# Performance work log

Hardware: AMD Instinct MI355X
Metric: run time of the kernel (lower is better)

## Reference

```python
import jax, jax.numpy as jnp
import numpy as np

B, DIN, DH, DOUT = 256, 784, 512, 10


def _softplus(x):
    # matches torch.log(1.0 + torch.exp(x)) exactly
    return jnp.log(1.0 + jnp.exp(x))


def _kl(w_mu, w_sigma_sp, size_in):
    # compute_kl_loss(w_mu, diag_embed(softplus(w_sigma))) without materializing diag
    # w_mu: (in, out), w_sigma_sp: (out, in)
    trace = jnp.sum(w_sigma_sp, axis=1)            # (out,)
    mu_sq = jnp.sum(w_mu * w_mu, axis=0)           # (out,)
    logdet = jnp.sum(jnp.log(w_sigma_sp), axis=1)  # slogdet of diag = sum log diag
    return 0.5 * jnp.sum(trace + mu_sq - size_in - logdet)


def setup_inputs() -> dict:
    key = jax.random.key(0)
    ks = jax.random.split(key, 9)
    inp = {
        "x": jax.random.normal(ks[0], (B, DIN, 1), dtype=jnp.float32),
        "w_mu1": 5e-5 * jax.random.normal(ks[1], (DIN, DH), dtype=jnp.float32),
        "w_sigma1": jax.random.uniform(ks[2], (DH, DIN), minval=-12.0, maxval=-2.0, dtype=jnp.float32),
        "b_mu1": 5e-5 * jax.random.normal(ks[3], (DH, 1), dtype=jnp.float32),
        "b_sigma1": jax.random.uniform(ks[4], (DH,), minval=-12.0, maxval=-2.0, dtype=jnp.float32),
        "w_mu2": 5e-5 * jax.random.normal(ks[5], (DH, DOUT), dtype=jnp.float32),
        "w_sigma2": jax.random.uniform(ks[6], (DOUT, DH), minval=-12.0, maxval=-2.0, dtype=jnp.float32),
        "b_mu2": 5e-5 * jax.random.normal(ks[7], (DOUT, 1), dtype=jnp.float32),
        "b_sigma2": jax.random.uniform(ks[8], (DOUT,), minval=-12.0, maxval=-2.0, dtype=jnp.float32),
    }
    return inp


def reference(x, w_mu1, w_sigma1, b_mu1, b_sigma1, w_mu2, w_sigma2, b_mu2, b_sigma2):
    batch = x.shape[0]
    eye_h = jnp.eye(DH, dtype=x.dtype)
    eye_o = jnp.eye(DOUT, dtype=x.dtype)

    # ---- RVLinearlayer 1 (sigma_in = None) ----
    xv = x[..., 0]                                   # (B, DIN)
    mu1 = jnp.einsum('io,bi->bo', w_mu1, xv)[:, :, None] + b_mu1   # (B, DH, 1)
    Ws1 = _softplus(w_sigma1)                        # (DH, DIN)
    quad1 = jnp.einsum('hi,bi->bh', Ws1, xv * xv)    # mu_in^T diag(Ws) mu_in per unit
    sigma1 = quad1[:, :, None] * eye_h + jnp.diag(_softplus(b_sigma1))  # (B, DH, DH)
    kl1 = _kl(w_mu1, Ws1, DIN)

    # ---- RVNonLinearFunc (ReLU) ----
    mu2 = jax.nn.relu(mu1)                           # (B, DH, 1)
    g = (mu1[..., 0] > 0).astype(x.dtype)            # Heaviside grad of relu
    sigma2 = sigma1 * (g[:, :, None] * g[:, None, :])

    # ---- RVLinearlayer 2 (with sigma_in) ----
    m2v = mu2[..., 0]                                # (B, DH)
    mu3 = jnp.einsum('ho,bh->bo', w_mu2, m2v)[:, :, None] + b_mu2   # (B, DOUT, 1)
    Ws2 = _softplus(w_sigma2)                        # (DOUT, DH)
    quad2 = jnp.einsum('oh,bh->bo', Ws2, m2v * m2v)  # (B, DOUT)
    # faithful replication of W_Sigma.view(out,-1) @ sigma_in.view(-1,B) then .view(B,out)
    Sflat = sigma2.reshape(DH * DH, batch)           # same row-major view as torch
    diag_rows = Sflat[jnp.arange(DH) * (DH + 1)]     # rows of the diag positions, (DH, B)
    tr = (Ws2 @ diag_rows).reshape(batch, DOUT)      # (out,B) -> row-major (B,out)
    mid = jnp.einsum('ho,bhk,kp->bop', w_mu2, sigma2, w_mu2)  # w_mu2^T Sigma w_mu2
    sigma3 = (tr[:, :, None] * eye_o + mid + quad2[:, :, None] * eye_o
              + jnp.diag(_softplus(b_sigma2)))       # (B, DOUT, DOUT)
    kl2 = _kl(w_mu2, Ws2, DH)

    # ---- RVSoftmax ----
    p = jax.nn.softmax(mu3[..., 0], axis=1)          # (B, DOUT)
    jac = p[:, :, None] * eye_o - p[:, :, None] * p[:, None, :]  # diag(p) - p p^T
    Sigma_out = jnp.einsum('bij,bjk,blk->bil', jac, sigma3, jac)

    return p, Sigma_out, kl1 + kl2
```

## Files before the change

kernel.cpp:

```cpp
#include <hip/hip_runtime.h>
#include <math.h>

#define BATCH 256
#define DIN 784
#define DH 512
#define DOUT 10
#define SPLITS 28
#define KSPL 28

__device__ __forceinline__ float softplus(float x) {
  return __logf(1.0f + __expf(x));
}

__global__ __launch_bounds__(256) void gemm1_kernel(
    const float* __restrict__ x, const float* __restrict__ w_mu1,
    const float* __restrict__ w_sigma1, const float* __restrict__ w_mu2,
    const float* __restrict__ w_sigma2, float* __restrict__ mu_part,
    float* __restrict__ q_part, float* __restrict__ kl_part) {
  __shared__ float xs[64][KSPL];
  __shared__ float wmt[KSPL][68];
  __shared__ float wst[KSPL][68];
  __shared__ float rlds[4];
  const int t = threadIdx.x;
  const int h0 = blockIdx.x * 64;
  const int b0 = blockIdx.y * 64;
  const int s = blockIdx.z;
  const int i0 = s * KSPL;
  const int hl = (t & 15) * 4;
  const int bg = (t >> 4) * 4;

  for (int f = t; f < 64 * KSPL; f += 256) {
    const int bb = f / KSPL, kk = f - bb * KSPL;
    xs[bb][kk] = x[(b0 + bb) * DIN + i0 + kk];
  }
  for (int f = t; f < KSPL * 64; f += 256) {
    const int kk = f >> 6, hh = f & 63;
    wmt[kk][hh] = w_mu1[(i0 + kk) * DH + h0 + hh];
  }
  for (int f = t; f < 64 * KSPL; f += 256) {
    const int hh = f / KSPL, kk = f - hh * KSPL;
    wst[kk][hh] = softplus(w_sigma1[(h0 + hh) * DIN + i0 + kk]);
  }
  __syncthreads();

  float mu[4][4], qq[4][4];
#pragma unroll
  for (int j = 0; j < 4; j++)
#pragma unroll
    for (int i = 0; i < 4; i++) {
      mu[j][i] = 0.f;
      qq[j][i] = 0.f;
    }

#pragma unroll 7
  for (int kk = 0; kk < KSPL; kk += 2) {
    const float4 wm0 = *(const float4*)&wmt[kk][hl];
    const float4 wm1 = *(const float4*)&wmt[kk + 1][hl];
    const float4 ws0 = *(const float4*)&wst[kk][hl];
    const float4 ws1 = *(const float4*)&wst[kk + 1][hl];
    const float* wm0a = (const float*)&wm0;
    const float* wm1a = (const float*)&wm1;
    const float* ws0a = (const float*)&ws0;
    const float* ws1a = (const float*)&ws1;
#pragma unroll
    for (int j = 0; j < 4; j++) {
      const float2 xv = *(const float2*)&xs[bg + j][kk];
      const float xx = xv.x, xy = xv.y;
      const float x2 = xx * xx, y2 = xy * xy;
#pragma unroll
      for (int i = 0; i < 4; i++) {
        mu[j][i] = fmaf(wm0a[i], xx, mu[j][i]);
        mu[j][i] = fmaf(wm1a[i], xy, mu[j][i]);
        qq[j][i] = fmaf(ws0a[i], x2, qq[j][i]);
        qq[j][i] = fmaf(ws1a[i], y2, qq[j][i]);
      }
    }
  }

  const int h = h0 + hl;
  const size_t base = (size_t)s * (BATCH * DH);
#pragma unroll
  for (int j = 0; j < 4; j++) {
    const size_t row = base + (size_t)(b0 + bg + j) * DH + h;
    *(float4*)&mu_part[row] =
        make_float4(mu[j][0], mu[j][1], mu[j][2], mu[j][3]);
    *(float4*)&q_part[row] =
        make_float4(qq[j][0], qq[j][1], qq[j][2], qq[j][3]);
  }

  float kl = 0.f;
  int slot = -1;
  if (blockIdx.y == 0) {
    for (int f = t; f < KSPL * 64; f += 256) {
      const int kk = f >> 6, hh = f & 63;
      const float sv = wst[kk][hh];
      kl += sv - __logf(sv);
    }
    slot = blockIdx.x * 28 + s;
  } else if (blockIdx.y == 1) {
    for (int f = t; f < KSPL * 64; f += 256) {
      const int kk = f >> 6, hh = f & 63;
      const float wv = wmt[kk][hh];
      kl = fmaf(wv, wv, kl);
    }
    slot = 224 + blockIdx.x * 28 + s;
  } else if (blockIdx.y == 2 && blockIdx.x == 0 && s < 16) {
    for (int idx = s * 320 + t; idx < s * 320 + 320; idx += 256) {
      const float sv = softplus(w_sigma2[idx]);
      const float wv = w_mu2[idx];
      kl += sv - __logf(sv);
      kl = fmaf(wv, wv, kl);
    }
    slot = 448 + s;
  }

  for (int off = 32; off > 0; off >>= 1) kl += __shfl_down(kl, off);
  const int lane = t & 63, wv = t >> 6;
  if (lane == 0) rlds[wv] = kl;
  __syncthreads();
  if (t == 0 && slot >= 0)
    kl_part[slot] = rlds[0] + rlds[1] + rlds[2] + rlds[3];
}

__global__ __launch_bounds__(512) void layer2_kernel(
    const float* __restrict__ mu_part, const float* __restrict__ q_part,
    const float* __restrict__ b_mu1, const float* __restrict__ b_sigma1,
    const float* __restrict__ w_mu2, const float* __restrict__ w_sigma2,
    const float* __restrict__ b_mu2, const float* __restrict__ b_sigma2,
    const float* __restrict__ kl_part, float* __restrict__ out_p,
    float* __restrict__ out_sigma, float* __restrict__ out_kl) {
  const int b = blockIdx.x, t = threadIdx.x;
  __shared__ float smuA[DH], sqA[DH], smuB[DH], sqB[DH];
  __shared__ float4 trp[10][7];
  __shared__ float red[8][75];
  __shared__ float fin[75];
  __shared__ float mu3[10], pvec[10], trv[10], spb2[10];
  __shared__ float sig[10][10], Tm[10][10], cs[10], rs[10];
  __shared__ float klred[8];

  {
    const int half = t >> 8;
    const int arr = (t >> 7) & 1;
    const int h4 = (t & 127) * 4;
    const float* srcbase = (arr == 0 ? mu_part : q_part);
    const float4* src = (const float4*)(srcbase + (size_t)b * DH + h4);
    float4 a = make_float4(0.f, 0.f, 0.f, 0.f);
#pragma unroll
    for (int s2 = half * 14; s2 < half * 14 + 14; s2++) {
      const float4 v = src[(size_t)s2 * (BATCH * DH / 4)];
      a.x += v.x;
      a.y += v.y;
      a.z += v.z;
      a.w += v.w;
    }
    float* dst = (half == 0 ? (arr == 0 ? smuA : sqA)
                            : (arr == 0 ? smuB : sqB));
    *(float4*)&dst[h4] = a;
  }

  if (t < 70) {
    const int o = t / 7, g = t % 7;
    const int cc = (b * 10 + o) & 255;
    float mua = 0.f, qa = 0.f, mub = 0.f, qb = 0.f;
#pragma unroll
    for (int s2 = 4 * g; s2 < 4 * g + 4; s2++) {
      const size_t base = (size_t)s2 * (BATCH * DH) + (size_t)cc * DH;
      mua += mu_part[base + cc];
      qa += q_part[base + cc];
      mub += mu_part[base + 256 + cc];
      qb += q_part[base + 256 + cc];
    }
    trp[o][g] = make_float4(mua, qa, mub, qb);
  }
  __syncthreads();

  const int h = t;
  float m2h, d2h;
  {
    const float ma = smuA[h] + smuB[h] + b_mu1[h];
    m2h = ma > 0.f ? ma : 0.f;
    d2h = ma > 0.f ? (sqA[h] + sqB[h] + softplus(b_sigma1[h])) : 0.f;
  }

  float acc[75];
#pragma unroll
  for (int i = 0; i < 75; i++) acc[i] = 0.f;
  {
    const float msq = m2h * m2h;
    float wrow[10];
#pragma unroll
    for (int o = 0; o < 10; o++) wrow[o] = w_mu2[h * 10 + o];
#pragma unroll
    for (int o = 0; o < 10; o++) {
      acc[o] = fmaf(wrow[o], m2h, acc[o]);
      acc[10 + o] = fmaf(softplus(w_sigma2[o * DH + h]), msq, acc[10 + o]);
    }
    int idx = 20;
#pragma unroll
    for (int o = 0; o < 10; o++) {
      const float wd = wrow[o] * d2h;
#pragma unroll
      for (int p = o; p < 10; p++) {
        acc[idx] = fmaf(wd, wrow[p], acc[idx]);
        idx++;
      }
    }
  }

  const int lane = t & 63, wv = t >> 6;
#pragma unroll
  for (int j = 0; j < 75; j++) {
    float v = acc[j];
    for (int off = 32; off > 0; off >>= 1) v += __shfl_down(v, off);
    if (lane == 0) red[wv][j] = v;
  }
  __syncthreads();
  if (t < 75) {
    float v = 0.f;
#pragma unroll
    for (int w = 0; w < 8; w++) v += red[w][t];
    fin[t] = v;
  }
  __syncthreads();

  if (t < 10) {
    mu3[t] = fin[t] + b_mu2[t];
    spb2[t] = softplus(b_sigma2[t]);
    const int c0 = b * 10 + t;
    const int o2 = c0 >> 8, cc = c0 & 255;
    float mua = b_mu1[cc], qa = 0.f;
    float mub = b_mu1[256 + cc], qb = 0.f;
#pragma unroll
    for (int g = 0; g < 7; g++) {
      const float4 v = trp[t][g];
      mua += v.x;
      qa += v.y;
      mub += v.z;
      qb += v.w;
    }
    const float d2aa = mua > 0.f ? (qa + softplus(b_sigma1[cc])) : 0.f;
    const float d2bb = mub > 0.f ? (qb + softplus(b_sigma1[256 + cc])) : 0.f;
    trv[t] = softplus(w_sigma2[o2 * DH + 2 * cc]) * d2aa +
             softplus(w_sigma2[o2 * DH + 2 * cc + 1]) * d2bb;
  }
  __syncthreads();

  if (t == 0) {
    float mx = mu3[0];
#pragma unroll
    for (int o = 1; o < 10; o++) mx = fmaxf(mx, mu3[o]);
    float e[10], se = 0.f;
#pragma unroll
    for (int o = 0; o < 10; o++) {
      e[o] = __expf(mu3[o] - mx);
      se += e[o];
    }
    const float inv = 1.f / se;
#pragma unroll
    for (int o = 0; o < 10; o++) pvec[o] = e[o] * inv;
  }
  __syncthreads();

  if (t < 100) {
    const int o = t / 10, p = t % 10;
    const int i0 = o < p ? o : p, j0 = o < p ? p : o;
    const int idx = 10 * i0 - (i0 * (i0 - 1)) / 2 + (j0 - i0);
    float v = fin[20 + idx];
    if (o == p) v += trv[o] + fin[10 + o] + spb2[o];
    sig[o][p] = v;
  }
  __syncthreads();

  if (t < 10) {
    float s = 0.f;
#pragma unroll
    for (int j = 0; j < 10; j++) s = fmaf(pvec[j], sig[j][t], s);
    cs[t] = s;
  }
  __syncthreads();

  if (t < 100) {
    const int o = t / 10, p = t % 10;
    Tm[o][p] = pvec[o] * (sig[o][p] - cs[p]);
  }
  __syncthreads();

  if (t < 10) {
    float s = 0.f;
#pragma unroll
    for (int k = 0; k < 10; k++) s = fmaf(Tm[t][k], pvec[k], s);
    rs[t] = s;
  }
  __syncthreads();

  if (t < 100) {
    const int o = t / 10, p = t % 10;
    out_sigma[b * 100 + t] = pvec[p] * (Tm[o][p] - rs[o]);
  }
  if (t < 10) out_p[b * 10 + t] = pvec[t];

  float klv = (b == 0 && t < 464) ? kl_part[t] : 0.f;
  for (int off = 32; off > 0; off >>= 1) klv += __shfl_down(klv, off);
  if (lane == 0) klred[wv] = klv;
  __syncthreads();
  if (b == 0 && t == 0) {
    float s = 0.f;
#pragma unroll
    for (int w = 0; w < 8; w++) s += klred[w];
    out_kl[0] = 0.5f * (s - 406528.0f);
  }
}

extern "C" void kernel_launch(void* const* d_in, const int* in_sizes, int n_in,
                              void* d_out, int out_size, void* d_ws,
                              size_t ws_size, hipStream_t stream) {
  const float* x = (const float*)d_in[0];
  const float* w_mu1 = (const float*)d_in[1];
  const float* w_sigma1 = (const float*)d_in[2];
  const float* b_mu1 = (const float*)d_in[3];
  const float* b_sigma1 = (const float*)d_in[4];
  const float* w_mu2 = (const float*)d_in[5];
  const float* w_sigma2 = (const float*)d_in[6];
  const float* b_mu2 = (const float*)d_in[7];
  const float* b_sigma2 = (const float*)d_in[8];

  float* out = (float*)d_out;
  float* out_p = out;
  float* out_sigma = out + 2560;
  float* out_kl = out + 28160;

  float* ws = (float*)d_ws;
  float* mu_part = ws;
  float* q_part = ws + SPLITS * BATCH * DH;
  float* kl_part = ws + 2 * SPLITS * BATCH * DH;

  gemm1_kernel<<<dim3(8, 4, SPLITS), 256, 0, stream>>>(
      x, w_mu1, w_sigma1, w_mu2, w_sigma2, mu_part, q_part, kl_part);
  layer2_kernel<<<256, 512, 0, stream>>>(mu_part, q_part, b_mu1, b_sigma1,
                                         w_mu2, w_sigma2, b_mu2, b_sigma2,
                                         kl_part, out_p, out_sigma, out_kl);
}
```

Before: 116.9 us.

## Retile GEMM1 to 64x128 tiles with 56 K-splits and re-slot KL partials

Doubles the batch tile per block to 128 rows, giving each thread 8x4 outputs, and halves the K chunk to 14 with 56 splits. This keeps 896 blocks while loading each softplus'd weight tile only twice instead of four times, so less weight traffic and softplus work is repeated. The cost is twice as many partial-sum buffers written and then read back in layer2, plus higher register pressure per thread. The KL partial slots are rearranged to match the new grid.

```diff
diff --git a/kernel.cpp b/kernel.cpp
--- a/kernel.cpp
+++ b/kernel.cpp
@@ -5,8 +5,8 @@
 #define DIN 784
 #define DH 512
 #define DOUT 10
-#define SPLITS 28
-#define KSPL 28
+#define SPLITS 56
+#define KSPL 14
 
 __device__ __forceinline__ float softplus(float x) {
   return __logf(1.0f + __expf(x));
@@ -17,19 +17,19 @@
     const float* __restrict__ w_sigma1, const float* __restrict__ w_mu2,
     const float* __restrict__ w_sigma2, float* __restrict__ mu_part,
     float* __restrict__ q_part, float* __restrict__ kl_part) {
-  __shared__ float xs[64][KSPL];
+  __shared__ float xs[128][KSPL];
   __shared__ float wmt[KSPL][68];
   __shared__ float wst[KSPL][68];
   __shared__ float rlds[4];
   const int t = threadIdx.x;
   const int h0 = blockIdx.x * 64;
-  const int b0 = blockIdx.y * 64;
+  const int b0 = blockIdx.y * 128;
   const int s = blockIdx.z;
   const int i0 = s * KSPL;
   const int hl = (t & 15) * 4;
-  const int bg = (t >> 4) * 4;
-
-  for (int f = t; f < 64 * KSPL; f += 256) {
+  const int bg = (t >> 4) * 8;
+
+  for (int f = t; f < 128 * KSPL; f += 256) {
     const int bb = f / KSPL, kk = f - bb * KSPL;
     xs[bb][kk] = x[(b0 + bb) * DIN + i0 + kk];
   }
@@ -43,16 +43,16 @@
   }
   __syncthreads();
 
-  float mu[4][4], qq[4][4];
-#pragma unroll
-  for (int j = 0; j < 4; j++)
+  float mu[8][4], qq[8][4];
+#pragma unroll
+  for (int j = 0; j < 8; j++)
 #pragma unroll
     for (int i = 0; i < 4; i++) {
       mu[j][i] = 0.f;
       qq[j][i] = 0.f;
     }
 
-#pragma unroll 7
+#pragma unroll
   for (int kk = 0; kk < KSPL; kk += 2) {
     const float4 wm0 = *(const float4*)&wmt[kk][hl];
     const float4 wm1 = *(const float4*)&wmt[kk + 1][hl];
@@ -63,7 +63,7 @@
     const float* ws0a = (const float*)&ws0;
     const float* ws1a = (const float*)&ws1;
 #pragma unroll
-    for (int j = 0; j < 4; j++) {
+    for (int j = 0; j < 8; j++) {
       const float2 xv = *(const float2*)&xs[bg + j][kk];
       const float xx = xv.x, xy = xv.y;
       const float x2 = xx * xx, y2 = xy * xy;
@@ -80,7 +80,7 @@
   const int h = h0 + hl;
   const size_t base = (size_t)s * (BATCH * DH);
 #pragma unroll
-  for (int j = 0; j < 4; j++) {
+  for (int j = 0; j < 8; j++) {
     const size_t row = base + (size_t)(b0 + bg + j) * DH + h;
     *(float4*)&mu_part[row] =
         make_float4(mu[j][0], mu[j][1], mu[j][2], mu[j][3]);
@@ -88,6 +88,7 @@
         make_float4(qq[j][0], qq[j][1], qq[j][2], qq[j][3]);
   }
 
+  const int lane = t & 63, wv = t >> 6;
   float kl = 0.f;
   int slot = -1;
   if (blockIdx.y == 0) {
@@ -96,30 +97,34 @@
       const float sv = wst[kk][hh];
       kl += sv - __logf(sv);
     }
-    slot = blockIdx.x * 28 + s;
-  } else if (blockIdx.y == 1) {
+    slot = blockIdx.x * 56 + s;
+  } else {
     for (int f = t; f < KSPL * 64; f += 256) {
       const int kk = f >> 6, hh = f & 63;
-      const float wv = wmt[kk][hh];
-      kl = fmaf(wv, wv, kl);
-    }
-    slot = 224 + blockIdx.x * 28 + s;
-  } else if (blockIdx.y == 2 && blockIdx.x == 0 && s < 16) {
+      const float wv2 = wmt[kk][hh];
+      kl = fmaf(wv2, wv2, kl);
+    }
+    slot = 448 + blockIdx.x * 56 + s;
+  }
+  for (int off = 32; off > 0; off >>= 1) kl += __shfl_down(kl, off);
+  if (lane == 0) rlds[wv] = kl;
+  __syncthreads();
+  if (t == 0) kl_part[slot] = rlds[0] + rlds[1] + rlds[2] + rlds[3];
+
+  if (blockIdx.y == 0 && blockIdx.x == 0 && s < 16) {
+    float kl2 = 0.f;
     for (int idx = s * 320 + t; idx < s * 320 + 320; idx += 256) {
       const float sv = softplus(w_sigma2[idx]);
-      const float wv = w_mu2[idx];
-      kl += sv - __logf(sv);
-      kl = fmaf(wv, wv, kl);
-    }
-    slot = 448 + s;
-  }
-
-  for (int off = 32; off > 0; off >>= 1) kl += __shfl_down(kl, off);
-  const int lane = t & 63, wv = t >> 6;
-  if (lane == 0) rlds[wv] = kl;
-  __syncthreads();
-  if (t == 0 && slot >= 0)
-    kl_part[slot] = rlds[0] + rlds[1] + rlds[2] + rlds[3];
+      const float wv2 = w_mu2[idx];
+      kl2 += sv - __logf(sv);
+      kl2 = fmaf(wv2, wv2, kl2);
+    }
+    for (int off = 32; off > 0; off >>= 1) kl2 += __shfl_down(kl2, off);
+    __syncthreads();
+    if (lane == 0) rlds[wv] = kl2;
+    __syncthreads();
+    if (t == 0) kl_part[896 + s] = rlds[0] + rlds[1] + rlds[2] + rlds[3];
+  }
 }
 
 __global__ __launch_bounds__(512) void layer2_kernel(
@@ -146,15 +151,15 @@
     const float4* src = (const float4*)(srcbase + (size_t)b * DH + h4);
     float4 a = make_float4(0.f, 0.f, 0.f, 0.f);
 #pragma unroll
-    for (int s2 = half * 14; s2 < half * 14 + 14; s2++) {
+    for (int s2 = half * 28; s2 < half * 28 + 28; s2++) {
       const float4 v = src[(size_t)s2 * (BATCH * DH / 4)];
       a.x += v.x;
       a.y += v.y;
       a.z += v.z;
       a.w += v.w;
     }
-    float* dst = (half == 0 ? (arr == 0 ? smuA : sqA)
-                            : (arr == 0 ? smuB : sqB));
+    float* dst =
+        (half == 0 ? (arr == 0 ? smuA : sqA) : (arr == 0 ? smuB : sqB));
     *(float4*)&dst[h4] = a;
   }
 
@@ -163,7 +168,7 @@
     const int cc = (b * 10 + o) & 255;
     float mua = 0.f, qa = 0.f, mub = 0.f, qb = 0.f;
 #pragma unroll
-    for (int s2 = 4 * g; s2 < 4 * g + 4; s2++) {
+    for (int s2 = 8 * g; s2 < 8 * g + 8; s2++) {
       const size_t base = (size_t)s2 * (BATCH * DH) + (size_t)cc * DH;
       mua += mu_part[base + cc];
       qa += q_part[base + cc];
@@ -299,7 +304,11 @@
   }
   if (t < 10) out_p[b * 10 + t] = pvec[t];
 
-  float klv = (b == 0 && t < 464) ? kl_part[t] : 0.f;
+  float klv = 0.f;
+  if (b == 0) {
+    klv = kl_part[t];
+    if (t < 400) klv += kl_part[512 + t];
+  }
   for (int off = 32; off > 0; off >>= 1) klv += __shfl_down(klv, off);
   if (lane == 0) klred[wv] = klv;
   __syncthreads();
@@ -334,7 +343,7 @@
   float* q_part = ws + SPLITS * BATCH * DH;
   float* kl_part = ws + 2 * SPLITS * BATCH * DH;
 
-  gemm1_kernel<<<dim3(8, 4, SPLITS), 256, 0, stream>>>(
+  gemm1_kernel<<<dim3(8, 2, SPLITS), 256, 0, stream>>>(
       x, w_mu1, w_sigma1, w_mu2, w_sigma2, mu_part, q_part, kl_part);
   layer2_kernel<<<256, 512, 0, stream>>>(mu_part, q_part, b_mu1, b_sigma1,
                                          w_mu2, w_sigma2, b_mu2, b_sigma2,
```

Measured after the change: 125.2 us. 1.07x slower.
